# Kernel optimization log

Measured on AMD Instinct MI355X. Metric: run time of the kernel, lower is better.

## Reference

```python
import jax, jax.numpy as jnp
import numpy as np

C = 64
CQ = C // 8
CR = C // 16  # SE reduction


def _conv1x1(x, W, b):
    # x: [B,C,V,T], W: [O,C], b: [O]
    return jnp.einsum('bcvt,oc->bovt', x, W) + b[None, :, None, None]


def setup_inputs() -> dict:
    key = jax.random.key(0)
    ks = jax.random.split(key, 10)
    B, V, T = 4, 224, 224
    s = 0.05
    return {
        'x': jax.random.normal(ks[0], (B, C, V, T), jnp.float32),
        'Wq': jax.random.normal(ks[1], (CQ, C), jnp.float32) * s,
        'bq': jax.random.normal(ks[2], (CQ,), jnp.float32) * s,
        'Wk': jax.random.normal(ks[3], (CQ, C), jnp.float32) * s,
        'bk': jax.random.normal(ks[4], (CQ,), jnp.float32) * s,
        'Wv': jax.random.normal(ks[5], (C, C), jnp.float32) * s,
        'bv': jax.random.normal(ks[6], (C,), jnp.float32) * s,
        'gamma': jax.random.normal(ks[7], (), jnp.float32) * 0.5,
        'W1': jax.random.normal(ks[8], (CR, C), jnp.float32) * s,
        'W2': jax.random.normal(ks[9], (C, CR), jnp.float32) * s,
    }


def reference(x, Wq, bq, Wk, bk, Wv, bv, gamma, W1, W2):
    B, Cc, V, T = x.shape
    # ---- CrissCrossAttention (add_input=True) ----
    q = _conv1x1(x, Wq, bq)  # [B,CQ,V,T]
    k = _conv1x1(x, Wk, bk)  # [B,CQ,V,T]
    v = _conv1x1(x, Wv, bv)  # [B,C,V,T]
    # column (H) attention: energy_H[b,v,t,u] = q[b,:,v,t].k[b,:,u,t], diag -inf
    energy_H = jnp.einsum('bcvt,bcut->bvtu', q, k)
    diag = jnp.eye(V, dtype=bool)[:, None, :]  # [V,1,V]
    energy_H = jnp.where(diag[None], -jnp.inf, energy_H)
    # row (W) attention: energy_W[b,v,t,s] = q[b,:,v,t].k[b,:,v,s]
    energy_W = jnp.einsum('bcvt,bcvs->bvts', q, k)
    concate = jax.nn.softmax(jnp.concatenate([energy_H, energy_W], axis=-1), axis=-1)
    att_H = concate[..., :V]       # [B,V,T,V]
    att_W = concate[..., V:V + T]  # [B,V,T,T]
    out_H = jnp.einsum('bcut,bvtu->bcvt', v, att_H)
    out_W = jnp.einsum('bcvs,bvts->bcvt', v, att_W)
    x1 = gamma * (out_H + out_W) + x
    # ---- SELayer (mul_input=True) ----
    y = jnp.mean(x, axis=(2, 3))                # [B,C]
    y = jax.nn.relu(jnp.einsum('bc,rc->br', y, W1))
    y = jax.nn.sigmoid(jnp.einsum('br,cr->bc', y, W2))
    x2 = x * y[:, :, None, None]
    # ---- structure == 'parallel' ----
    return x1 + x2
```

## Files before the change

### kernel.cpp

```cpp
#include <hip/hip_runtime.h>
#include <math.h>

#define CC 64
#define CQv 8
#define CRv 4
#define BB 4
#define RR 224
#define TT 224
#define NN (RR*TT)
#define LOG2E 1.4426950408889634f

typedef __attribute__((ext_vector_type(8))) short short8;
typedef __attribute__((ext_vector_type(4))) float f32x4;

__device__ __forceinline__ f32x4 mfma_bf16(short8 a, short8 b, f32x4 c){
    return __builtin_amdgcn_mfma_f32_16x16x32_bf16(a, b, c, 0, 0, 0);
}

__device__ __forceinline__ ushort f2bf(float f){
    union { float f; unsigned u; } v; v.f = f;
    unsigned r = v.u + 0x7fffu + ((v.u >> 16) & 1u);
    return (ushort)(r >> 16);
}
__device__ __forceinline__ float bf2f(ushort u){
    return __uint_as_float((unsigned)u << 16);
}
__device__ __forceinline__ unsigned packbf(float a, float b){
    return __builtin_amdgcn_perm(__float_as_uint(b), __float_as_uint(a), 0x07060302u);
}
__device__ __forceinline__ int vswz(int row, int uslot){
    return (uslot ^ (row & 7) ^ ((row >> 3) & 7)) << 4;
}

__global__ __launch_bounds__(256) void k_qkv(
    const float* __restrict__ x,
    const float* __restrict__ Wq, const float* __restrict__ bq,
    const float* __restrict__ Wk, const float* __restrict__ bk,
    const float* __restrict__ Wv, const float* __restrict__ bv,
    ushort* __restrict__ qB, ushort* __restrict__ kB, ushort* __restrict__ vB,
    float* __restrict__ partial)
{
    const int tid = threadIdx.x;
    const int w = tid >> 6, l = tid & 63, l15 = l & 15, lg = l >> 4;
    const int blk = blockIdx.x;
    const int b = blk / 196, pb = blk - b*196;
    const int n0 = pb*256;
    const float* xb = x + (size_t)b*CC*NN;

    short8 afr[5][2];
#pragma unroll
    for (int ot = 0; ot < 5; ++ot) {
        int oo = ot*16 + l15;
        const float* wr = (oo < 8) ? (Wq + oo*64)
                        : (oo < 16) ? (Wk + (oo-8)*64)
                                    : (Wv + (oo-16)*64);
        float scl = (oo >= 8 && oo < 16) ? LOG2E : 1.0f;
#pragma unroll
        for (int ks = 0; ks < 2; ++ks) {
            const float* p = wr + ks*32 + lg*8;
            float4 w0 = *(const float4*)p, w1 = *(const float4*)(p+4);
            short8 f;
            f[0]=f2bf(w0.x*scl); f[1]=f2bf(w0.y*scl); f[2]=f2bf(w0.z*scl); f[3]=f2bf(w0.w*scl);
            f[4]=f2bf(w1.x*scl); f[5]=f2bf(w1.y*scl); f[6]=f2bf(w1.z*scl); f[7]=f2bf(w1.w*scl);
            afr[ot][ks] = f;
        }
    }
    f32x4 binit[5];
#pragma unroll
    for (int ot = 0; ot < 5; ++ot) {
        const float* bp;
        float scl = 1.0f;
        if (ot == 0) { bp = (lg < 2) ? (bq + lg*4) : (bk + (lg-2)*4); if (lg >= 2) scl = LOG2E; }
        else           bp = bv + (ot-1)*16 + lg*4;
        float4 bb4 = *(const float4*)bp;
        binit[ot] = (f32x4){bb4.x*scl, bb4.y*scl, bb4.z*scl, bb4.w*scl};
    }

    float msum[16];
#pragma unroll
    for (int i = 0; i < 16; ++i) msum[i] = 0.f;

#pragma unroll
    for (int j = 0; j < 4; ++j) {
        int n = n0 + (w*4 + j)*16 + l15;
        short8 bfr[2];
#pragma unroll
        for (int ks = 0; ks < 2; ++ks) {
            const float* xp = xb + (size_t)(ks*32 + lg*8)*NN + n;
            short8 f;
#pragma unroll
            for (int e = 0; e < 8; ++e) {
                float xv = xp[(size_t)e*NN];
                f[e] = f2bf(xv);
                msum[ks*8 + e] += xv;
            }
            bfr[ks] = f;
        }
#pragma unroll
        for (int ot = 0; ot < 5; ++ot) {
            f32x4 acc = binit[ot];
            acc = mfma_bf16(afr[ot][0], bfr[0], acc);
            acc = mfma_bf16(afr[ot][1], bfr[1], acc);
            ushort4 pk;
            pk.x = f2bf(acc[0]); pk.y = f2bf(acc[1]);
            pk.z = f2bf(acc[2]); pk.w = f2bf(acc[3]);
            if (ot == 0) {
                ushort* dst = (lg < 2) ? (qB + ((size_t)b*NN + n)*8 + lg*4)
                                       : (kB + ((size_t)b*NN + n)*8 + (lg-2)*4);
                *(ushort4*)dst = pk;
            } else {
                int oc = (ot-1)*16 + lg*4;
                *(ushort4*)(vB + ((size_t)b*NN + n)*64 + oc) = pk;
            }
        }
    }

#pragma unroll
    for (int i = 0; i < 16; ++i) {
        float s = msum[i];
        s += __shfl_xor(s, 1); s += __shfl_xor(s, 2);
        s += __shfl_xor(s, 4); s += __shfl_xor(s, 8);
        msum[i] = s;
    }
    __shared__ float msums[4][4][16];
    if (l15 == 0) {
#pragma unroll
        for (int i = 0; i < 16; ++i) msums[w][lg][i] = msum[i];
    }
    __syncthreads();
    if (tid < 64) {
        int c = tid;
        int lgi = (c >> 3) & 3, ii = (c >> 5)*8 + (c & 7);
        float t = msums[0][lgi][ii] + msums[1][lgi][ii] + msums[2][lgi][ii] + msums[3][lgi][ii];
        partial[(size_t)blk*64 + c] = t;
    }
}

__global__ __launch_bounds__(256) void k_tq(const uint4* __restrict__ qs, const uint4* __restrict__ ks,
                                            uint4* __restrict__ qd, uint4* __restrict__ kd)
{
    __shared__ uint4 tile[32][33];
    int z = blockIdx.z;
    int b = z & 3;
    const uint4* sp = ((z >= 4) ? ks : qs) + (size_t)b*NN;
    uint4*       dp = ((z >= 4) ? kd : qd) + (size_t)b*NN;
    int t0 = blockIdx.x*32, r0 = blockIdx.y*32;
    int tx = threadIdx.x & 31, ty = threadIdx.x >> 5;
#pragma unroll
    for (int j = 0; j < 4; ++j) { int lr = ty + 8*j; tile[lr][tx] = sp[(size_t)(r0+lr)*224 + t0 + tx]; }
    __syncthreads();
#pragma unroll
    for (int j = 0; j < 4; ++j) { int lt = ty + 8*j; dp[(size_t)(t0+lt)*224 + r0 + tx] = tile[tx][lt]; }
}

__global__ __launch_bounds__(256, 3) void k_pv(const ushort* __restrict__ qA, const ushort* __restrict__ kA,
                                               const ushort* __restrict__ qB, const ushort* __restrict__ kB,
                                               const ushort* __restrict__ vB,
                                               ushort* __restrict__ outA, ushort* __restrict__ outB,
                                               float* __restrict__ ZHt, float* __restrict__ ZWt)
{
    __shared__ __align__(16) ushort Vt[64*256];
    __shared__ __align__(16) ushort Ah[32*256];
    __shared__ float zred[4][32];

    const int tid = threadIdx.x;
    const int bid = blockIdx.x;
    const bool HM = bid < BB*224;
    const int blk = HM ? bid : bid - BB*224;
    const int b = blk / 224, o = blk - b*224;
    const ushort* Qsrc = (HM ? qA : qB) + (size_t)blk*1792;
    const ushort* Ksrc = (HM ? kA : kB) + (size_t)blk*1792;
    ushort* op = (HM ? outA : outB) + (size_t)blk*14336;
    float*  Zt = (HM ? ZHt : ZWt) + (size_t)blk*224;

    {
        const uint4* vbase = (const uint4*)vB;
        for (int gi = tid; gi < 448; gi += 256) {
            int ublk = gi >> 3, sub = gi & 7;
            int u0 = ublk << 2;
            size_t base, stride;
            if (HM) { base = ((size_t)b*NN + (size_t)u0*224 + o)*8 + sub; stride = 1792; }
            else    { base = ((size_t)blk*224 + u0)*8 + sub;              stride = 8;    }
            uint4 r0 = vbase[base], r1 = vbase[base+stride], r2 = vbase[base+2*stride], r3 = vbase[base+3*stride];
            const ushort* p0 = (const ushort*)&r0;
            const ushort* p1 = (const ushort*)&r1;
            const ushort* p2 = (const ushort*)&r2;
            const ushort* p3 = (const ushort*)&r3;
            int half = (ublk & 1) * 8;
#pragma unroll
            for (int j = 0; j < 8; ++j) {
                int c = sub*8 + j;
                ushort4 col; col.x = p0[j]; col.y = p1[j]; col.z = p2[j]; col.w = p3[j];
                *(ushort4*)((char*)Vt + c*512 + vswz(c, ublk >> 1) + half) = col;
            }
        }
    }
    __syncthreads();

    const int w = tid >> 6, l = tid & 63;
    const int l15 = l & 15, lg = l >> 4;
    const short8 zfr = {0,0,0,0,0,0,0,0};
    const f32x4 zacc = {0.f,0.f,0.f,0.f};

    short8 vfr[7];
    {
        int c = w*16 + l15;
#pragma unroll
        for (int ks = 0; ks < 7; ++ks)
            vfr[ks] = *(const short8*)((const char*)Vt + c*512 + vswz(c, ks*4 + lg));
    }
    short8 kf[4];
#pragma unroll
    for (int j = 0; j < 4; ++j) {
        int ut = w + 4*j;
        kf[j] = (ut < 14 && lg == 0) ? *(const short8*)(Ksrc + (size_t)(ut*16 + l15)*8) : zfr;
    }

    for (int ch = 0; ch < 7; ++ch) {
        const int r0 = ch*32;
        {
            short8 qf[2];
            float zp[2] = {0.f, 0.f};
#pragma unroll
            for (int rt = 0; rt < 2; ++rt) {
                int r = r0 + rt*16 + l15;
                qf[rt] = (lg == 0) ? *(const short8*)(Qsrc + (size_t)r*8) : zfr;
            }
#pragma unroll
            for (int j = 0; j < 4; ++j) {
                int ut = w + 4*j;
                if (ut < 14) {
#pragma unroll
                    for (int rt = 0; rt < 2; ++rt) {
                        f32x4 e = mfma_bf16(kf[j], qf[rt], zacc);
                        int ubase = ut*16 + lg*4;
                        int r = r0 + rt*16 + l15;
                        float a0 = __builtin_amdgcn_exp2f(e[0]);
                        float a1 = __builtin_amdgcn_exp2f(e[1]);
                        float a2 = __builtin_amdgcn_exp2f(e[2]);
                        float a3 = __builtin_amdgcn_exp2f(e[3]);
                        if (HM) {
                            if (ubase+0 == r) a0 = 0.f;
                            if (ubase+1 == r) a1 = 0.f;
                            if (ubase+2 == r) a2 = 0.f;
                            if (ubase+3 == r) a3 = 0.f;
                        }
                        zp[rt] += (a0 + a1) + (a2 + a3);
                        int rl = rt*16 + l15;
                        uint2 pk; pk.x = packbf(a0, a1); pk.y = packbf(a2, a3);
                        *(uint2*)((char*)Ah + rl*512 + vswz(rl, ut*2 + (lg >> 1)) + (lg & 1)*8) = pk;
                    }
                }
            }
#pragma unroll
            for (int rt = 0; rt < 2; ++rt) {
                float z = zp[rt];
                z += __shfl_xor(z, 16);
                z += __shfl_xor(z, 32);
                if (lg == 0) zred[w][rt*16 + l15] = z;
            }
        }
        __syncthreads();
        if (tid < 32)
            Zt[r0 + tid] = (zred[0][tid] + zred[1][tid]) + (zred[2][tid] + zred[3][tid]);
        {
#pragma unroll
            for (int rt = 0; rt < 2; ++rt) {
                f32x4 acc = zacc;
                int rl = rt*16 + l15;
#pragma unroll
                for (int ks = 0; ks < 7; ++ks) {
                    short8 af = *(const short8*)((const char*)Ah + rl*512 + vswz(rl, ks*4 + lg));
                    acc = mfma_bf16(vfr[ks], af, acc);
                }
                int c0 = w*16 + lg*4;
                int r = r0 + rl;
#pragma unroll
                for (int reg = 0; reg < 4; ++reg)
                    op[(size_t)(c0+reg)*224 + r] = f2bf(acc[reg]);
            }
        }
        __syncthreads();
    }
}

__global__ __launch_bounds__(256) void k_aux(const float* __restrict__ ZHt, const float* __restrict__ ZWt,
                                             const float* __restrict__ gammap,
                                             const float* __restrict__ partial,
                                             const float* __restrict__ W1, const float* __restrict__ W2,
                                             float* __restrict__ Zi, float* __restrict__ y2)
{
    const int blk = blockIdx.x;
    if (blk < 196) {
        __shared__ float tile[32][33];
        int b = blk / 49, rem = blk - b*49;
        int t0 = (rem % 7)*32, v0 = (rem / 7)*32;
        int tx = threadIdx.x & 31, ty = threadIdx.x >> 5;
        float g = gammap[0];
#pragma unroll
        for (int j = 0; j < 4; ++j) {
            int tl = ty + 8*j;
            tile[tl][tx] = ZHt[((size_t)(b*224 + t0 + tl))*224 + v0 + tx];
        }
        __syncthreads();
#pragma unroll
        for (int j = 0; j < 4; ++j) {
            int vl = ty + 8*j;
            size_t i = ((size_t)(b*224 + v0 + vl))*224 + t0 + tx;
            float zs = tile[tx][vl] + ZWt[i];
            Zi[i] = g * __builtin_amdgcn_rcpf(zs);
        }
    } else {
        __shared__ float mean_s[4][64];
        int tid = threadIdx.x;
        int b = tid >> 6, c = tid & 63;
        float s = 0.f;
        for (int i = 0; i < 196; ++i) s += partial[((size_t)(b*196 + i))*64 + c];
        mean_s[b][c] = s * (1.0f/NN);
        __syncthreads();
        float h[CRv];
#pragma unroll
        for (int j = 0; j < CRv; ++j) {
            float t = 0.f;
#pragma unroll
            for (int cc = 0; cc < CC; ++cc) t += W1[j*CC + cc] * mean_s[b][cc];
            h[j] = fmaxf(t, 0.f);
        }
        float s2 = 0.f;
#pragma unroll
        for (int j = 0; j < CRv; ++j) s2 += W2[c*CRv + j] * h[j];
        y2[tid] = 1.f/(1.f + __expf(-s2));
    }
}

__global__ __launch_bounds__(256) void k_final(const float* __restrict__ x,
                                               const ushort* __restrict__ outA,
                                               const ushort* __restrict__ outB,
                                               const float* __restrict__ Zi,
                                               const float* __restrict__ y2,
                                               float* __restrict__ out)
{
    __shared__ ushort tile[32][34];
    int bc = blockIdx.z;
    int b = bc >> 6, c = bc & 63;
    int t0 = blockIdx.x*32, r0 = blockIdx.y*32;
    int tx = threadIdx.x & 31, ty = threadIdx.x >> 5;
    float scale = 1.f + y2[bc];
#pragma unroll
    for (int j = 0; j < 4; ++j) {
        int tl = ty + 8*j;
        tile[tl][tx] = outA[((size_t)(b*224 + t0 + tl)*64 + c)*224 + r0 + tx];
    }
    __syncthreads();
#pragma unroll
    for (int j = 0; j < 4; ++j) {
        int rl = ty + 8*j;
        size_t pidx = (size_t)(r0 + rl)*224 + t0 + tx;
        size_t idx = (size_t)bc*NN + pidx;
        float a = bf2f(tile[tx][rl]);
        float wv = bf2f(outB[((size_t)(b*224 + r0 + rl)*64 + c)*224 + t0 + tx]);
        float zi = Zi[(size_t)b*NN + pidx];
        out[idx] = x[idx]*scale + (a + wv)*zi;
    }
}

extern "C" void kernel_launch(void* const* d_in, const int* in_sizes, int n_in,
                              void* d_out, int out_size, void* d_ws, size_t ws_size,
                              hipStream_t stream)
{
    const float* x  = (const float*)d_in[0];
    const float* Wq = (const float*)d_in[1];
    const float* bq = (const float*)d_in[2];
    const float* Wk = (const float*)d_in[3];
    const float* bk = (const float*)d_in[4];
    const float* Wv = (const float*)d_in[5];
    const float* bv = (const float*)d_in[6];
    const float* gm = (const float*)d_in[7];
    const float* W1 = (const float*)d_in[8];
    const float* W2 = (const float*)d_in[9];
    float* out = (float*)d_out;

    constexpr size_t QSZ = (size_t)BB*NN*CQv;
    constexpr size_t VSZ = (size_t)BB*NN*CC;
    constexpr size_t SSZ = (size_t)BB*NN;

    ushort* qB = (ushort*)d_ws;
    ushort* kB = qB + QSZ;
    ushort* vB = kB + QSZ;
    ushort* qA = vB + VSZ;
    ushort* kA = qA + QSZ;
    ushort* outA = kA + QSZ;
    ushort* outB = outA + VSZ;
    float*  ZHt = (float*)(outB + VSZ);
    float*  ZWt = ZHt + SSZ;
    float*  Zi  = ZWt + SSZ;
    float*  partial = Zi + SSZ;
    float*  y2 = partial + (size_t)BB*196*64;
    (void)ws_size; (void)in_sizes; (void)n_in; (void)out_size;

    k_qkv<<<BB*196, 256, 0, stream>>>(x, Wq, bq, Wk, bk, Wv, bv, qB, kB, vB, partial);
    k_tq<<<dim3(7,7,8), 256, 0, stream>>>((const uint4*)qB, (const uint4*)kB, (uint4*)qA, (uint4*)kA);

    k_pv<<<2*BB*224, 256, 0, stream>>>(qA, kA, qB, kB, vB, outA, outB, ZHt, ZWt);
    k_aux<<<197, 256, 0, stream>>>(ZHt, ZWt, gm, partial, W1, W2, Zi, y2);

    k_final<<<dim3(7,7,BB*CC), 256, 0, stream>>>(x, outA, outB, Zi, y2, out);
}
```

Baseline: 120.0 us.

## Keep attention probabilities in registers via bpermute, drop LDS staging and barriers

Restructures the k_pv kernel so each wavefront owns whole 16-row chunks. It computes energies against K staged in LDS, exponentiates, and reshuffles the bf16 probabilities into MFMA A-operand layout with ds_bpermute rather than writing them to a shared Ah buffer. This removes the Ah and zred shared arrays and the per-chunk __syncthreads pairs, and it lets the occupancy hint rise from 3 to 4 blocks. V fragments are reloaded from LDS inside the loop instead of kept in registers, and the 14 chunks spread unevenly across 4 waves.

```diff
diff --git a/kernel.cpp b/kernel.cpp
--- a/kernel.cpp
+++ b/kernel.cpp
@@ -153,15 +153,14 @@
     for (int j = 0; j < 4; ++j) { int lt = ty + 8*j; dp[(size_t)(t0+lt)*224 + r0 + tx] = tile[tx][lt]; }
 }
 
-__global__ __launch_bounds__(256, 3) void k_pv(const ushort* __restrict__ qA, const ushort* __restrict__ kA,
+__global__ __launch_bounds__(256, 4) void k_pv(const ushort* __restrict__ qA, const ushort* __restrict__ kA,
                                                const ushort* __restrict__ qB, const ushort* __restrict__ kB,
                                                const ushort* __restrict__ vB,
                                                ushort* __restrict__ outA, ushort* __restrict__ outB,
                                                float* __restrict__ ZHt, float* __restrict__ ZWt)
 {
     __shared__ __align__(16) ushort Vt[64*256];
-    __shared__ __align__(16) ushort Ah[32*256];
-    __shared__ float zred[4][32];
+    __shared__ __align__(16) ushort Kh[224*8];
 
     const int tid = threadIdx.x;
     const int bid = blockIdx.x;
@@ -195,6 +194,7 @@
             }
         }
     }
+    if (tid < 224) ((uint4*)Kh)[tid] = ((const uint4*)Ksrc)[tid];
     __syncthreads();
 
     const int w = tid >> 6, l = tid & 63;
@@ -202,85 +202,72 @@
     const short8 zfr = {0,0,0,0,0,0,0,0};
     const f32x4 zacc = {0.f,0.f,0.f,0.f};
 
-    short8 vfr[7];
-    {
-        int c = w*16 + l15;
-#pragma unroll
-        for (int ks = 0; ks < 7; ++ks)
-            vfr[ks] = *(const short8*)((const char*)Vt + c*512 + vswz(c, ks*4 + lg));
-    }
-    short8 kf[4];
-#pragma unroll
-    for (int j = 0; j < 4; ++j) {
-        int ut = w + 4*j;
-        kf[j] = (ut < 14 && lg == 0) ? *(const short8*)(Ksrc + (size_t)(ut*16 + l15)*8) : zfr;
-    }
-
-    for (int ch = 0; ch < 7; ++ch) {
-        const int r0 = ch*32;
+    const int src0 = (l15 + ((lg & 1) << 5)) << 2;
+    const int src1 = src0 + 64;
+    const bool hi = (lg >= 2);
+
+    for (int ch = w; ch < 14; ch += 4) {
+        short8 qf = zfr;
+        if (lg == 0) qf = *(const short8*)(Qsrc + (size_t)(ch*16 + l15)*8);
+        f32x4 acc0 = zacc, acc1 = zacc, acc2 = zacc, acc3 = zacc;
+        float zsum = 0.f;
+#pragma unroll
+        for (int ks = 0; ks < 7; ++ks) {
+            short8 kf0 = *(const short8*)(Kh + (size_t)(ks*32 + l15)*8);
+            short8 kf1 = *(const short8*)(Kh + (size_t)(ks*32 + 16 + l15)*8);
+            f32x4 e0 = mfma_bf16(kf0, qf, zacc);
+            f32x4 e1 = mfma_bf16(kf1, qf, zacc);
+            float a0[4], a1[4];
+#pragma unroll
+            for (int g = 0; g < 4; ++g) {
+                a0[g] = __builtin_amdgcn_exp2f(e0[g]);
+                a1[g] = __builtin_amdgcn_exp2f(e1[g]);
+            }
+            if (HM && (ch >> 1) == ks) {
+                if ((ch & 1) == 0) {
+#pragma unroll
+                    for (int g = 0; g < 4; ++g) if (lg*4 + g == l15) a0[g] = 0.f;
+                } else {
+#pragma unroll
+                    for (int g = 0; g < 4; ++g) if (lg*4 + g == l15) a1[g] = 0.f;
+                }
+            }
+            zsum += ((a0[0]+a0[1]) + (a0[2]+a0[3])) + ((a1[0]+a1[1]) + (a1[2]+a1[3]));
+            unsigned p00 = packbf(a0[0], a0[1]), p01 = packbf(a0[2], a0[3]);
+            unsigned p10 = packbf(a1[0], a1[1]), p11 = packbf(a1[2], a1[3]);
+            unsigned s0 = hi ? p10 : p00;
+            unsigned s1 = hi ? p11 : p01;
+            int fx = __builtin_amdgcn_ds_bpermute(src0, (int)s0);
+            int fy = __builtin_amdgcn_ds_bpermute(src0, (int)s1);
+            int fz = __builtin_amdgcn_ds_bpermute(src1, (int)s0);
+            int fw = __builtin_amdgcn_ds_bpermute(src1, (int)s1);
+            int4 fi; fi.x = fx; fi.y = fy; fi.z = fz; fi.w = fw;
+            short8 af = *(short8*)&fi;
+            {
+                short8 vf0 = *(const short8*)((const char*)Vt + (size_t)(l15)*512       + vswz(l15,      ks*4 + lg));
+                short8 vf1 = *(const short8*)((const char*)Vt + (size_t)(16 + l15)*512  + vswz(16 + l15, ks*4 + lg));
+                short8 vf2 = *(const short8*)((const char*)Vt + (size_t)(32 + l15)*512  + vswz(32 + l15, ks*4 + lg));
+                short8 vf3 = *(const short8*)((const char*)Vt + (size_t)(48 + l15)*512  + vswz(48 + l15, ks*4 + lg));
+                acc0 = mfma_bf16(af, vf0, acc0);
+                acc1 = mfma_bf16(af, vf1, acc1);
+                acc2 = mfma_bf16(af, vf2, acc2);
+                acc3 = mfma_bf16(af, vf3, acc3);
+            }
+        }
+        zsum += __shfl_xor(zsum, 16);
+        zsum += __shfl_xor(zsum, 32);
+        if (lg == 0) Zt[ch*16 + l15] = zsum;
         {
-            short8 qf[2];
-            float zp[2] = {0.f, 0.f};
-#pragma unroll
-            for (int rt = 0; rt < 2; ++rt) {
-                int r = r0 + rt*16 + l15;
-                qf[rt] = (lg == 0) ? *(const short8*)(Qsrc + (size_t)r*8) : zfr;
-            }
-#pragma unroll
-            for (int j = 0; j < 4; ++j) {
-                int ut = w + 4*j;
-                if (ut < 14) {
-#pragma unroll
-                    for (int rt = 0; rt < 2; ++rt) {
-                        f32x4 e = mfma_bf16(kf[j], qf[rt], zacc);
-                        int ubase = ut*16 + lg*4;
-                        int r = r0 + rt*16 + l15;
-                        float a0 = __builtin_amdgcn_exp2f(e[0]);
-                        float a1 = __builtin_amdgcn_exp2f(e[1]);
-                        float a2 = __builtin_amdgcn_exp2f(e[2]);
-                        float a3 = __builtin_amdgcn_exp2f(e[3]);
-                        if (HM) {
-                            if (ubase+0 == r) a0 = 0.f;
-                            if (ubase+1 == r) a1 = 0.f;
-                            if (ubase+2 == r) a2 = 0.f;
-                            if (ubase+3 == r) a3 = 0.f;
-                        }
-                        zp[rt] += (a0 + a1) + (a2 + a3);
-                        int rl = rt*16 + l15;
-                        uint2 pk; pk.x = packbf(a0, a1); pk.y = packbf(a2, a3);
-                        *(uint2*)((char*)Ah + rl*512 + vswz(rl, ut*2 + (lg >> 1)) + (lg & 1)*8) = pk;
-                    }
-                }
-            }
-#pragma unroll
-            for (int rt = 0; rt < 2; ++rt) {
-                float z = zp[rt];
-                z += __shfl_xor(z, 16);
-                z += __shfl_xor(z, 32);
-                if (lg == 0) zred[w][rt*16 + l15] = z;
-            }
-        }
-        __syncthreads();
-        if (tid < 32)
-            Zt[r0 + tid] = (zred[0][tid] + zred[1][tid]) + (zred[2][tid] + zred[3][tid]);
-        {
-#pragma unroll
-            for (int rt = 0; rt < 2; ++rt) {
-                f32x4 acc = zacc;
-                int rl = rt*16 + l15;
-#pragma unroll
-                for (int ks = 0; ks < 7; ++ks) {
-                    short8 af = *(const short8*)((const char*)Ah + rl*512 + vswz(rl, ks*4 + lg));
-                    acc = mfma_bf16(vfr[ks], af, acc);
-                }
-                int c0 = w*16 + lg*4;
-                int r = r0 + rl;
-#pragma unroll
-                for (int reg = 0; reg < 4; ++reg)
-                    op[(size_t)(c0+reg)*224 + r] = f2bf(acc[reg]);
-            }
-        }
-        __syncthreads();
+            int rbase = ch*16 + lg*4;
+            f32x4 av[4] = {acc0, acc1, acc2, acc3};
+#pragma unroll
+            for (int ct = 0; ct < 4; ++ct) {
+                ushort4 pk;
+                pk.x = f2bf(av[ct][0]); pk.y = f2bf(av[ct][1]);
+                pk.z = f2bf(av[ct][2]); pk.w = f2bf(av[ct][3]);
+                *(ushort4*)(op + (size_t)(ct*16 + l15)*224 + rbase) = pk;
+            }
+        }
     }
 }
 
```

After: 278.2 us. +131.9%, slower.
